# Kernel optimization log

Hardware: AMD Instinct MI355X
Metric: run time of the kernel (lower is better)

## Reference

```python
import jax, jax.numpy as jnp
import numpy as np

N_NODES = 10000
N_EDGES = 320000
D = 256
VOCAB = 28
NEG_SLOPE = 0.2


def _gat_conv(x, ei_src, ei_dst, W, a_src, a_dst, b):
    """PyG GATConv with heads=1, concat=True, self-loops already in ei."""
    h = x @ W                                  # [N, D]
    alpha_s = h @ a_src                        # [N]
    alpha_d = h @ a_dst                        # [N]
    logits = jax.nn.leaky_relu(alpha_s[ei_src] + alpha_d[ei_dst], NEG_SLOPE)  # [E]
    # numerically stable edge softmax per destination node
    m = jax.ops.segment_max(logits, ei_dst, num_segments=N_NODES)
    e = jnp.exp(logits - m[ei_dst])
    denom = jax.ops.segment_sum(e, ei_dst, num_segments=N_NODES)
    alpha = e / denom[ei_dst]                  # [E]
    msgs = alpha[:, None] * h[ei_src]          # [E, D]
    out = jax.ops.segment_sum(msgs, ei_dst, num_segments=N_NODES)
    return out + b


def setup_inputs() -> dict:
    key = jax.random.key(0)
    ks = jax.random.split(key, 16)
    x = jax.random.randint(ks[0], (N_NODES, 1), 0, VOCAB, dtype=jnp.int64)
    edge_index = jax.random.randint(ks[1], (2, N_EDGES), 0, N_NODES, dtype=jnp.int64)
    edge_attr = jax.random.uniform(ks[2], (N_EDGES,), dtype=jnp.float32)
    sc = 1.0 / np.sqrt(D)
    inp = {"x": x, "edge_index": edge_index, "edge_attr": edge_attr,
           "emb": jax.random.normal(ks[3], (VOCAB, D), jnp.float32)}
    for i, k0 in enumerate([4, 7, 10]):
        l = i + 1
        inp[f"W{l}"] = jax.random.normal(ks[k0], (D, D), jnp.float32) * sc
        inp[f"a_src{l}"] = jax.random.normal(ks[k0 + 1], (D,), jnp.float32) * sc
        inp[f"a_dst{l}"] = jax.random.normal(ks[k0 + 2], (D,), jnp.float32) * sc
        inp[f"b{l}"] = jnp.zeros((D,), jnp.float32)
    return inp


def reference(x, edge_index, edge_attr, emb,
              W1, a_src1, a_dst1, b1,
              W2, a_src2, a_dst2, b2,
              W3, a_src3, a_dst3, b3):
    # edge_attr is ignored by GATConv (edge_dim=None), matching PyG behavior.
    # add self loops (PyG default add_self_loops=True)
    loops = jnp.arange(N_NODES, dtype=edge_index.dtype)
    ei_src = jnp.concatenate([edge_index[0], loops])
    ei_dst = jnp.concatenate([edge_index[1], loops])

    h = emb[x.squeeze(-1)]                     # [N, D]
    h = jax.nn.relu(_gat_conv(h, ei_src, ei_dst, W1, a_src1, a_dst1, b1)) + h
    h = jax.nn.relu(_gat_conv(h, ei_src, ei_dst, W2, a_src2, a_dst2, b2)) + h
    out = jax.nn.relu(_gat_conv(h, ei_src, ei_dst, W3, a_src3, a_dst3, b3)) + h
    return out
```

## Files before the change

kernel.cpp:

```cpp
#include <hip/hip_runtime.h>
#include <hip/hip_bf16.h>

#define N_NODES 10000
#define N_EDGES 320000
#define E_TOT (N_EDGES + N_NODES)
#define D 256
#define VOCAB 28
#define NEG 0.2f
#define CAP 96

typedef __attribute__((ext_vector_type(8))) short bf16x8;
typedef __attribute__((ext_vector_type(4))) float f32x4;

__device__ inline float blo(unsigned u) { return __uint_as_float(u << 16); }
__device__ inline float bhi(unsigned u) { return __uint_as_float(u & 0xFFFF0000u); }
__device__ inline unsigned short f2bu(float x) {
  __hip_bfloat16 b = __float2bfloat16(x);
  return *reinterpret_cast<unsigned short*>(&b);
}

__global__ __launch_bounds__(256) void prep_kernel(const float* __restrict__ W0,
                                                   const float* __restrict__ W1,
                                                   const float* __restrict__ W2,
                                                   const float* __restrict__ emb,
                                                   const float* __restrict__ as1,
                                                   const float* __restrict__ ad1,
                                                   const float* __restrict__ as2,
                                                   const float* __restrict__ ad2,
                                                   const float* __restrict__ as3,
                                                   const float* __restrict__ ad3,
                                                   const int* __restrict__ x,
                                                   unsigned short* __restrict__ T0,
                                                   unsigned short* __restrict__ T1,
                                                   unsigned short* __restrict__ T2,
                                                   unsigned short* __restrict__ emb_b,
                                                   float4* __restrict__ zbase,
                                                   float* __restrict__ waS2,
                                                   float* __restrict__ waD2,
                                                   float* __restrict__ waS3,
                                                   float* __restrict__ waD3,
                                                   float* __restrict__ al1_s,
                                                   float* __restrict__ al1_d) {
  int tid = threadIdx.x;
  int bid = blockIdx.x;
  if (bid < 48) {
    __shared__ float t[64][65];
    int l = bid >> 4;
    const float* W = (l == 0) ? W0 : (l == 1) ? W1 : W2;
    unsigned short* Wt = (l == 0) ? T0 : (l == 1) ? T1 : T2;
    int sub = bid & 15;
    int bk = (sub & 3) * 64;
    int bn = (sub >> 2) * 64;
    int row = tid >> 2;
    int cq = (tid & 3) * 16;
#pragma unroll
    for (int i = 0; i < 4; ++i) {
      float4 v = *reinterpret_cast<const float4*>(W + (size_t)(bk + row) * D + bn + cq + i * 4);
      t[row][cq + i * 4 + 0] = v.x; t[row][cq + i * 4 + 1] = v.y;
      t[row][cq + i * 4 + 2] = v.z; t[row][cq + i * 4 + 3] = v.w;
    }
    __syncthreads();
#pragma unroll
    for (int i = 0; i < 16; ++i)
      Wt[(size_t)(bn + row) * D + bk + cq + i] = f2bu(t[cq + i][row]);
  } else if (bid == 48) {
    for (int i = tid; i < VOCAB * D; i += 256) emb_b[i] = f2bu(emb[i]);
  } else if (bid < 59) {
    zbase[(bid - 49) * 256 + tid] = float4{0.f, 0.f, 0.f, 0.f};
  } else if (bid == 59 || bid == 60) {
    const float* W = (bid == 59) ? W1 : W2;
    const float* as = (bid == 59) ? as2 : as3;
    const float* ad = (bid == 59) ? ad2 : ad3;
    float* oS = (bid == 59) ? waS2 : waS3;
    float* oD = (bid == 59) ? waD2 : waD3;
    float s = 0.f, d = 0.f;
    const float* row = W + (size_t)tid * D;
    for (int n = 0; n < D; ++n) {
      float w = row[n];
      s += w * as[n];
      d += w * ad[n];
    }
    oS[tid] = s; oD[tid] = d;
  } else {
    __shared__ float ws1[256], wd1[256], avs[VOCAB], avd[VOCAB];
    {
      float s = 0.f, d = 0.f;
      const float* row = W0 + (size_t)tid * D;
      for (int n = 0; n < D; ++n) {
        float w = row[n];
        s += w * as1[n];
        d += w * ad1[n];
      }
      ws1[tid] = s; wd1[tid] = d;
    }
    __syncthreads();
    int wid = tid >> 6, lane = tid & 63;
    for (int t = wid; t < VOCAB; t += 4) {
      float ps = 0.f, pd = 0.f;
      for (int k = lane; k < D; k += 64) {
        float e = emb[(size_t)t * D + k];
        ps += e * ws1[k];
        pd += e * wd1[k];
      }
#pragma unroll
      for (int off = 32; off; off >>= 1) {
        ps += __shfl_xor(ps, off);
        pd += __shfl_xor(pd, off);
      }
      if (lane == 0) { avs[t] = ps; avd[t] = pd; }
    }
    __syncthreads();
    for (int n = tid; n < N_NODES; n += 256) {
      int t = x[n];
      al1_s[n] = avs[t];
      al1_d[n] = avd[t];
    }
  }
}

__global__ __launch_bounds__(256) void scatter_kernel(const int* __restrict__ ei,
                                                      int* __restrict__ counts,
                                                      int* __restrict__ csr) {
  int e = blockIdx.x * 256 + threadIdx.x;
  if (e >= E_TOT) return;
  int src, dst;
  if (e < N_EDGES) { src = ei[e]; dst = ei[N_EDGES + e]; }
  else             { src = e - N_EDGES; dst = src; }
  int pos = atomicAdd(&counts[dst], 1);
  csr[dst * CAP + pos] = src;
}

__global__ __launch_bounds__(256) void gemm_kernel(const unsigned short* __restrict__ Asrc,
                                                   const int* __restrict__ xv,
                                                   const unsigned short* __restrict__ emb_b,
                                                   const unsigned short* __restrict__ Bt,
                                                   unsigned short* __restrict__ C) {
  __shared__ unsigned short As[64][72];
  __shared__ unsigned short Bs[64][72];
  __shared__ int xs[64];
  int t = threadIdx.x;
  int bm = blockIdx.x * 64;
  int bn = blockIdx.y * 64;
  int lane = t & 63, wid = t >> 6;
  int wr = (wid >> 1) * 32, wc = (wid & 1) * 32;
  int fr = lane & 15, fk = (lane >> 4) * 8;

  if (xv) {
    if (t < 64) {
      int gr = bm + t;
      xs[t] = (gr < N_NODES) ? xv[gr] : 0;
    }
    __syncthreads();
  }

  f32x4 acc[2][2] = {};
  for (int k0 = 0; k0 < D; k0 += 64) {
#pragma unroll
    for (int c = t; c < 512; c += 256) {
      int row = c >> 3, cc = (c & 7) * 8;
      int gr = bm + row;
      uint4 v = {0u, 0u, 0u, 0u};
      if (gr < N_NODES) {
        const unsigned short* src = xv ? (emb_b + (size_t)xs[row] * D)
                                       : (Asrc + (size_t)gr * D);
        v = *reinterpret_cast<const uint4*>(src + k0 + cc);
      }
      *reinterpret_cast<uint4*>(&As[row][cc]) = v;
      uint4 w = *reinterpret_cast<const uint4*>(Bt + (size_t)(bn + row) * D + k0 + cc);
      *reinterpret_cast<uint4*>(&Bs[row][cc]) = w;
    }
    __syncthreads();
#pragma unroll
    for (int ks = 0; ks < 2; ++ks) {
      bf16x8 a0 = *reinterpret_cast<const bf16x8*>(&As[wr + fr][ks * 32 + fk]);
      bf16x8 a1 = *reinterpret_cast<const bf16x8*>(&As[wr + 16 + fr][ks * 32 + fk]);
      bf16x8 b0 = *reinterpret_cast<const bf16x8*>(&Bs[wc + fr][ks * 32 + fk]);
      bf16x8 b1 = *reinterpret_cast<const bf16x8*>(&Bs[wc + 16 + fr][ks * 32 + fk]);
      acc[0][0] = __builtin_amdgcn_mfma_f32_16x16x32_bf16(a0, b0, acc[0][0], 0, 0, 0);
      acc[0][1] = __builtin_amdgcn_mfma_f32_16x16x32_bf16(a0, b1, acc[0][1], 0, 0, 0);
      acc[1][0] = __builtin_amdgcn_mfma_f32_16x16x32_bf16(a1, b0, acc[1][0], 0, 0, 0);
      acc[1][1] = __builtin_amdgcn_mfma_f32_16x16x32_bf16(a1, b1, acc[1][1], 0, 0, 0);
    }
    __syncthreads();
  }

  int orow = (lane >> 4) * 4;
#pragma unroll
  for (int m = 0; m < 2; ++m)
#pragma unroll
    for (int n = 0; n < 2; ++n)
#pragma unroll
      for (int r = 0; r < 4; ++r) {
        int gr = bm + wr + m * 16 + orow + r;
        if (gr < N_NODES)
          C[(size_t)gr * D + bn + wc + n * 16 + fr] = f2bu(acc[m][n][r]);
      }
}

__global__ __launch_bounds__(256) void agg_kernel(const int* __restrict__ csr,
                                                  const int* __restrict__ counts,
                                                  const float* __restrict__ al_s,
                                                  const float* __restrict__ al_d,
                                                  const unsigned short* __restrict__ hlin,
                                                  const float* __restrict__ bias,
                                                  const float* __restrict__ h_prev,
                                                  const int* __restrict__ xv,
                                                  const float* __restrict__ emb,
                                                  float* __restrict__ out_f,
                                                  unsigned short* __restrict__ out_b,
                                                  const float* __restrict__ waS_n,
                                                  const float* __restrict__ waD_n,
                                                  float* __restrict__ aln_s,
                                                  float* __restrict__ aln_d) {
  __shared__ int   ssh[4][CAP];
  __shared__ float wsh[4][CAP];
  int wid = threadIdx.x >> 6, lane = threadIdx.x & 63;
  int dst = blockIdx.x * 4 + wid;
  if (dst >= N_NODES) return;
  int cnt = counts[dst];
  const int* rowp = csr + (size_t)dst * CAP;
  float ad = al_d[dst];

  float m = -1e30f;
  for (int j = lane; j < cnt; j += 64) {
    int s = rowp[j];
    ssh[wid][j] = s;
    float v = al_s[s] + ad;
    v = (v >= 0.f) ? v : NEG * v;
    wsh[wid][j] = v;
    m = fmaxf(m, v);
  }
#pragma unroll
  for (int off = 32; off; off >>= 1) m = fmaxf(m, __shfl_xor(m, off));

  float denom = 0.f;
  for (int j = lane; j < cnt; j += 64) {
    float w = __expf(wsh[wid][j] - m);
    wsh[wid][j] = w;
    denom += w;
  }
#pragma unroll
  for (int off = 32; off; off >>= 1) denom += __shfl_xor(denom, off);
  float inv = 1.0f / denom;

  int half = lane >> 5, fl = lane & 31;
  const unsigned short* hb_base = hlin + fl * 8;
  float a0 = 0.f, a1 = 0.f, a2 = 0.f, a3 = 0.f;
  float a4 = 0.f, a5 = 0.f, a6 = 0.f, a7 = 0.f;
  int j = 0;
  for (; j + 8 <= cnt; j += 8) {
    int s0 = ssh[wid][j + 0 + half];
    int s1 = ssh[wid][j + 2 + half];
    int s2 = ssh[wid][j + 4 + half];
    int s3 = ssh[wid][j + 6 + half];
    float w0 = wsh[wid][j + 0 + half];
    float w1 = wsh[wid][j + 2 + half];
    float w2 = wsh[wid][j + 4 + half];
    float w3 = wsh[wid][j + 6 + half];
    uint4 q0 = *reinterpret_cast<const uint4*>(hb_base + (size_t)s0 * D);
    uint4 q1 = *reinterpret_cast<const uint4*>(hb_base + (size_t)s1 * D);
    uint4 q2 = *reinterpret_cast<const uint4*>(hb_base + (size_t)s2 * D);
    uint4 q3 = *reinterpret_cast<const uint4*>(hb_base + (size_t)s3 * D);
    a0 += w0 * blo(q0.x); a1 += w0 * bhi(q0.x); a2 += w0 * blo(q0.y); a3 += w0 * bhi(q0.y);
    a4 += w0 * blo(q0.z); a5 += w0 * bhi(q0.z); a6 += w0 * blo(q0.w); a7 += w0 * bhi(q0.w);
    a0 += w1 * blo(q1.x); a1 += w1 * bhi(q1.x); a2 += w1 * blo(q1.y); a3 += w1 * bhi(q1.y);
    a4 += w1 * blo(q1.z); a5 += w1 * bhi(q1.z); a6 += w1 * blo(q1.w); a7 += w1 * bhi(q1.w);
    a0 += w2 * blo(q2.x); a1 += w2 * bhi(q2.x); a2 += w2 * blo(q2.y); a3 += w2 * bhi(q2.y);
    a4 += w2 * blo(q2.z); a5 += w2 * bhi(q2.z); a6 += w2 * blo(q2.w); a7 += w2 * bhi(q2.w);
    a0 += w3 * blo(q3.x); a1 += w3 * bhi(q3.x); a2 += w3 * blo(q3.y); a3 += w3 * bhi(q3.y);
    a4 += w3 * blo(q3.z); a5 += w3 * bhi(q3.z); a6 += w3 * blo(q3.w); a7 += w3 * bhi(q3.w);
  }
  for (; j < cnt; j += 2) {
    int jj = j + half;
    bool valid = jj < cnt;
    int s0 = ssh[wid][valid ? jj : 0];
    float w0 = valid ? wsh[wid][jj] : 0.f;
    uint4 q0 = *reinterpret_cast<const uint4*>(hb_base + (size_t)s0 * D);
    a0 += w0 * blo(q0.x); a1 += w0 * bhi(q0.x); a2 += w0 * blo(q0.y); a3 += w0 * bhi(q0.y);
    a4 += w0 * blo(q0.z); a5 += w0 * bhi(q0.z); a6 += w0 * blo(q0.w); a7 += w0 * bhi(q0.w);
  }
  a0 += __shfl_xor(a0, 32); a1 += __shfl_xor(a1, 32);
  a2 += __shfl_xor(a2, 32); a3 += __shfl_xor(a3, 32);
  a4 += __shfl_xor(a4, 32); a5 += __shfl_xor(a5, 32);
  a6 += __shfl_xor(a6, 32); a7 += __shfl_xor(a7, 32);
  float b0 = half ? a4 : a0, b1 = half ? a5 : a1;
  float b2 = half ? a6 : a2, b3 = half ? a7 : a3;
  int fb = fl * 8 + half * 4;
  const float* hp_row = h_prev ? (h_prev + (size_t)dst * D)
                               : (emb + (size_t)xv[dst] * D);
  float4 bb = *reinterpret_cast<const float4*>(bias + fb);
  float4 hp = *reinterpret_cast<const float4*>(hp_row + fb);
  float o0 = fmaxf(b0 * inv + bb.x, 0.f) + hp.x;
  float o1 = fmaxf(b1 * inv + bb.y, 0.f) + hp.y;
  float o2 = fmaxf(b2 * inv + bb.z, 0.f) + hp.z;
  float o3 = fmaxf(b3 * inv + bb.w, 0.f) + hp.w;
  float4 o = {o0, o1, o2, o3};
  *reinterpret_cast<float4*>(out_f + (size_t)dst * D + fb) = o;
  if (out_b) {
    uint2 p;
    p.x = (unsigned)f2bu(o0) | ((unsigned)f2bu(o1) << 16);
    p.y = (unsigned)f2bu(o2) | ((unsigned)f2bu(o3) << 16);
    *reinterpret_cast<uint2*>(out_b + (size_t)dst * D + fb) = p;
  }
  if (waS_n) {
    float4 s4 = *reinterpret_cast<const float4*>(waS_n + fb);
    float4 d4 = *reinterpret_cast<const float4*>(waD_n + fb);
    float ps = o0 * s4.x + o1 * s4.y + o2 * s4.z + o3 * s4.w;
    float pd = o0 * d4.x + o1 * d4.y + o2 * d4.z + o3 * d4.w;
#pragma unroll
    for (int off = 32; off; off >>= 1) {
      ps += __shfl_xor(ps, off);
      pd += __shfl_xor(pd, off);
    }
    if (lane == 0) { aln_s[dst] = ps; aln_d[dst] = pd; }
  }
}

extern "C" void kernel_launch(void* const* d_in, const int* in_sizes, int n_in,
                              void* d_out, int out_size, void* d_ws, size_t ws_size,
                              hipStream_t stream) {
  const int*   x   = (const int*)d_in[0];
  const int*   ei  = (const int*)d_in[1];
  const float* emb = (const float*)d_in[3];
  const float* W[3]    = {(const float*)d_in[4],  (const float*)d_in[8],  (const float*)d_in[12]};
  const float* asrc[3] = {(const float*)d_in[5],  (const float*)d_in[9],  (const float*)d_in[13]};
  const float* adst[3] = {(const float*)d_in[6],  (const float*)d_in[10], (const float*)d_in[14]};
  const float* bias[3] = {(const float*)d_in[7],  (const float*)d_in[11], (const float*)d_in[15]};

  char* ws = (char*)d_ws;
  float*          h    = (float*)(ws);
  unsigned short* hb   = (unsigned short*)(ws + 10240000);
  unsigned short* hlin = (unsigned short*)(ws + 15360000);
  unsigned short* Wt[3] = {(unsigned short*)(ws + 20480000),
                           (unsigned short*)(ws + 20611072),
                           (unsigned short*)(ws + 20742144)};
  float* al_s[3] = {(float*)(ws + 20873216), (float*)(ws + 20914176), (float*)(ws + 20955136)};
  float* al_d[3] = {(float*)(ws + 20996096), (float*)(ws + 21037056), (float*)(ws + 21078016)};
  int* counts = (int*)(ws + 21118976);
  int* csr    = (int*)(ws + 21241856);
  unsigned short* emb_b = (unsigned short*)(ws + 25081856);
  float* waS2 = (float*)(ws + 25096192);
  float* waD2 = (float*)(ws + 25097216);
  float* waS3 = (float*)(ws + 25098240);
  float* waD3 = (float*)(ws + 25099264);

  prep_kernel<<<62, 256, 0, stream>>>(W[0], W[1], W[2], emb,
                                      asrc[0], adst[0], asrc[1], adst[1], asrc[2], adst[2],
                                      x, Wt[0], Wt[1], Wt[2], emb_b,
                                      (float4*)counts, waS2, waD2, waS3, waD3,
                                      al_s[0], al_d[0]);

  scatter_kernel<<<(E_TOT + 255) / 256, 256, 0, stream>>>(ei, counts, csr);

  dim3 gemm_grid(157, 4);
  for (int l = 0; l < 3; ++l) {
    const unsigned short* Ain = (l == 0) ? (const unsigned short*)nullptr : hb;
    const int* xg = (l == 0) ? x : (const int*)nullptr;
    gemm_kernel<<<gemm_grid, 256, 0, stream>>>(Ain, xg, emb_b, Wt[l], hlin);
    float* outp = (l == 2) ? (float*)d_out : h;
    unsigned short* outb = (l == 2) ? (unsigned short*)nullptr : hb;
    const float* hp = (l == 0) ? (const float*)nullptr : h;
    const float* wsn = (l == 0) ? waS2 : (l == 1) ? waS3 : (const float*)nullptr;
    const float* wdn = (l == 0) ? waD2 : (l == 1) ? waD3 : (const float*)nullptr;
    float* alns = (l < 2) ? al_s[l + 1] : (float*)nullptr;
    float* alnd = (l < 2) ? al_d[l + 1] : (float*)nullptr;
    agg_kernel<<<(N_NODES + 3) / 4, 256, 0, stream>>>(csr, counts, al_s[l], al_d[l],
                                                      hlin, bias[l], hp, x, emb,
                                                      outp, outb, wsn, wdn, alns, alnd);
  }
}
```

Baseline: 135.1 us.

## Aggregate before linear transform and fuse GEMM with residual and attention epilogue

Uses linearity of the attention-weighted sum to swap the order of work in each layer. Each layer now aggregates the bf16 input features first, and in layer one it gathers straight from the 28-row embedding table. A single full-width GEMM per 64-row tile then applies bias, ReLU and the residual, and computes the next layer's attention projections in its epilogue. The goals are cache-friendly gathers in the first layer and no round trip of the separate linear output through memory. In exchange the GEMM runs with only 157 blocks, uses large LDS tiles and writes scalar outputs, and the rounding order of the bf16 steps changes.

```diff
diff --git a/kernel.cpp b/kernel.cpp
--- a/kernel.cpp
+++ b/kernel.cpp
@@ -130,88 +130,13 @@
   csr[dst * CAP + pos] = src;
 }
 
-__global__ __launch_bounds__(256) void gemm_kernel(const unsigned short* __restrict__ Asrc,
+__global__ __launch_bounds__(256) void aggz_kernel(const int* __restrict__ csr,
+                                                   const int* __restrict__ counts,
+                                                   const float* __restrict__ al_s,
+                                                   const float* __restrict__ al_d,
+                                                   const unsigned short* __restrict__ table,
                                                    const int* __restrict__ xv,
-                                                   const unsigned short* __restrict__ emb_b,
-                                                   const unsigned short* __restrict__ Bt,
-                                                   unsigned short* __restrict__ C) {
-  __shared__ unsigned short As[64][72];
-  __shared__ unsigned short Bs[64][72];
-  __shared__ int xs[64];
-  int t = threadIdx.x;
-  int bm = blockIdx.x * 64;
-  int bn = blockIdx.y * 64;
-  int lane = t & 63, wid = t >> 6;
-  int wr = (wid >> 1) * 32, wc = (wid & 1) * 32;
-  int fr = lane & 15, fk = (lane >> 4) * 8;
-
-  if (xv) {
-    if (t < 64) {
-      int gr = bm + t;
-      xs[t] = (gr < N_NODES) ? xv[gr] : 0;
-    }
-    __syncthreads();
-  }
-
-  f32x4 acc[2][2] = {};
-  for (int k0 = 0; k0 < D; k0 += 64) {
-#pragma unroll
-    for (int c = t; c < 512; c += 256) {
-      int row = c >> 3, cc = (c & 7) * 8;
-      int gr = bm + row;
-      uint4 v = {0u, 0u, 0u, 0u};
-      if (gr < N_NODES) {
-        const unsigned short* src = xv ? (emb_b + (size_t)xs[row] * D)
-                                       : (Asrc + (size_t)gr * D);
-        v = *reinterpret_cast<const uint4*>(src + k0 + cc);
-      }
-      *reinterpret_cast<uint4*>(&As[row][cc]) = v;
-      uint4 w = *reinterpret_cast<const uint4*>(Bt + (size_t)(bn + row) * D + k0 + cc);
-      *reinterpret_cast<uint4*>(&Bs[row][cc]) = w;
-    }
-    __syncthreads();
-#pragma unroll
-    for (int ks = 0; ks < 2; ++ks) {
-      bf16x8 a0 = *reinterpret_cast<const bf16x8*>(&As[wr + fr][ks * 32 + fk]);
-      bf16x8 a1 = *reinterpret_cast<const bf16x8*>(&As[wr + 16 + fr][ks * 32 + fk]);
-      bf16x8 b0 = *reinterpret_cast<const bf16x8*>(&Bs[wc + fr][ks * 32 + fk]);
-      bf16x8 b1 = *reinterpret_cast<const bf16x8*>(&Bs[wc + 16 + fr][ks * 32 + fk]);
-      acc[0][0] = __builtin_amdgcn_mfma_f32_16x16x32_bf16(a0, b0, acc[0][0], 0, 0, 0);
-      acc[0][1] = __builtin_amdgcn_mfma_f32_16x16x32_bf16(a0, b1, acc[0][1], 0, 0, 0);
-      acc[1][0] = __builtin_amdgcn_mfma_f32_16x16x32_bf16(a1, b0, acc[1][0], 0, 0, 0);
-      acc[1][1] = __builtin_amdgcn_mfma_f32_16x16x32_bf16(a1, b1, acc[1][1], 0, 0, 0);
-    }
-    __syncthreads();
-  }
-
-  int orow = (lane >> 4) * 4;
-#pragma unroll
-  for (int m = 0; m < 2; ++m)
-#pragma unroll
-    for (int n = 0; n < 2; ++n)
-#pragma unroll
-      for (int r = 0; r < 4; ++r) {
-        int gr = bm + wr + m * 16 + orow + r;
-        if (gr < N_NODES)
-          C[(size_t)gr * D + bn + wc + n * 16 + fr] = f2bu(acc[m][n][r]);
-      }
-}
-
-__global__ __launch_bounds__(256) void agg_kernel(const int* __restrict__ csr,
-                                                  const int* __restrict__ counts,
-                                                  const float* __restrict__ al_s,
-                                                  const float* __restrict__ al_d,
-                                                  const unsigned short* __restrict__ hlin,
-                                                  const float* __restrict__ bias,
-                                                  const float* __restrict__ h_prev,
-                                                  const int* __restrict__ xv,
-                                                  const float* __restrict__ emb,
-                                                  float* __restrict__ out_f,
-                                                  unsigned short* __restrict__ out_b,
-                                                  const float* __restrict__ waS_n,
-                                                  const float* __restrict__ waD_n,
-                                                  float* __restrict__ aln_s,
-                                                  float* __restrict__ aln_d) {
+                                                   unsigned short* __restrict__ zb) {
   __shared__ int   ssh[4][CAP];
   __shared__ float wsh[4][CAP];
   int wid = threadIdx.x >> 6, lane = threadIdx.x & 63;
@@ -224,9 +149,9 @@
   float m = -1e30f;
   for (int j = lane; j < cnt; j += 64) {
     int s = rowp[j];
-    ssh[wid][j] = s;
     float v = al_s[s] + ad;
     v = (v >= 0.f) ? v : NEG * v;
+    ssh[wid][j] = xv ? xv[s] : s;
     wsh[wid][j] = v;
     m = fmaxf(m, v);
   }
@@ -244,7 +169,7 @@
   float inv = 1.0f / denom;
 
   int half = lane >> 5, fl = lane & 31;
-  const unsigned short* hb_base = hlin + fl * 8;
+  const unsigned short* hb_base = table + fl * 8;
   float a0 = 0.f, a1 = 0.f, a2 = 0.f, a3 = 0.f;
   float a4 = 0.f, a5 = 0.f, a6 = 0.f, a7 = 0.f;
   int j = 0;
@@ -286,33 +211,132 @@
   float b0 = half ? a4 : a0, b1 = half ? a5 : a1;
   float b2 = half ? a6 : a2, b3 = half ? a7 : a3;
   int fb = fl * 8 + half * 4;
-  const float* hp_row = h_prev ? (h_prev + (size_t)dst * D)
-                               : (emb + (size_t)xv[dst] * D);
-  float4 bb = *reinterpret_cast<const float4*>(bias + fb);
-  float4 hp = *reinterpret_cast<const float4*>(hp_row + fb);
-  float o0 = fmaxf(b0 * inv + bb.x, 0.f) + hp.x;
-  float o1 = fmaxf(b1 * inv + bb.y, 0.f) + hp.y;
-  float o2 = fmaxf(b2 * inv + bb.z, 0.f) + hp.z;
-  float o3 = fmaxf(b3 * inv + bb.w, 0.f) + hp.w;
-  float4 o = {o0, o1, o2, o3};
-  *reinterpret_cast<float4*>(out_f + (size_t)dst * D + fb) = o;
-  if (out_b) {
-    uint2 p;
-    p.x = (unsigned)f2bu(o0) | ((unsigned)f2bu(o1) << 16);
-    p.y = (unsigned)f2bu(o2) | ((unsigned)f2bu(o3) << 16);
-    *reinterpret_cast<uint2*>(out_b + (size_t)dst * D + fb) = p;
-  }
+  uint2 p;
+  p.x = (unsigned)f2bu(b0 * inv) | ((unsigned)f2bu(b1 * inv) << 16);
+  p.y = (unsigned)f2bu(b2 * inv) | ((unsigned)f2bu(b3 * inv) << 16);
+  *reinterpret_cast<uint2*>(zb + (size_t)dst * D + fb) = p;
+}
+
+__global__ __launch_bounds__(256) void gemmf_kernel(const unsigned short* __restrict__ Az,
+                                                    const unsigned short* __restrict__ Bt,
+                                                    const float* __restrict__ bias,
+                                                    const float* __restrict__ h_prev,
+                                                    const int* __restrict__ xv,
+                                                    const float* __restrict__ emb,
+                                                    float* __restrict__ h_out,
+                                                    unsigned short* __restrict__ hb_out,
+                                                    const float* __restrict__ waS_n,
+                                                    const float* __restrict__ waD_n,
+                                                    float* __restrict__ aln_s,
+                                                    float* __restrict__ aln_d) {
+  __shared__ unsigned short As[64][264];
+  __shared__ unsigned short Bs[64][264];
+  __shared__ float red_s[8][32];
+  __shared__ float red_d[8][32];
+  __shared__ int xs[64];
+  int t = threadIdx.x;
+  int bm = blockIdx.x * 64;
+  int lane = t & 63, wid = t >> 6;
+  int wrb = (wid >> 1) * 32, wcb = (wid & 1) * 32;
+  int fr = lane & 15, fk = (lane >> 4) * 8;
+  int orow = (lane >> 4) * 4;
+
+  if (xv) {
+    if (t < 64) {
+      int gr = bm + t;
+      xs[t] = (gr < N_NODES) ? xv[gr] : 0;
+    }
+    __syncthreads();
+  }
+
+#pragma unroll
+  for (int c = t; c < 2048; c += 256) {
+    int row = c >> 5, cc = (c & 31) * 8;
+    int gr = bm + row;
+    uint4 v = {0u, 0u, 0u, 0u};
+    if (gr < N_NODES)
+      v = *reinterpret_cast<const uint4*>(Az + (size_t)gr * D + cc);
+    *reinterpret_cast<uint4*>(&As[row][cc]) = v;
+  }
+
+  float aS[2][4] = {}, aD[2][4] = {};
+  for (int bn = 0; bn < 4; ++bn) {
+#pragma unroll
+    for (int c = t; c < 2048; c += 256) {
+      int row = c >> 5, cc = (c & 31) * 8;
+      uint4 w = *reinterpret_cast<const uint4*>(Bt + (size_t)(bn * 64 + row) * D + cc);
+      *reinterpret_cast<uint4*>(&Bs[row][cc]) = w;
+    }
+    __syncthreads();
+
+    f32x4 acc[2][2] = {};
+#pragma unroll
+    for (int ks = 0; ks < 8; ++ks) {
+      bf16x8 a0 = *reinterpret_cast<const bf16x8*>(&As[wrb + fr][ks * 32 + fk]);
+      bf16x8 a1 = *reinterpret_cast<const bf16x8*>(&As[wrb + 16 + fr][ks * 32 + fk]);
+      bf16x8 b0 = *reinterpret_cast<const bf16x8*>(&Bs[wcb + fr][ks * 32 + fk]);
+      bf16x8 b1 = *reinterpret_cast<const bf16x8*>(&Bs[wcb + 16 + fr][ks * 32 + fk]);
+      acc[0][0] = __builtin_amdgcn_mfma_f32_16x16x32_bf16(a0, b0, acc[0][0], 0, 0, 0);
+      acc[0][1] = __builtin_amdgcn_mfma_f32_16x16x32_bf16(a0, b1, acc[0][1], 0, 0, 0);
+      acc[1][0] = __builtin_amdgcn_mfma_f32_16x16x32_bf16(a1, b0, acc[1][0], 0, 0, 0);
+      acc[1][1] = __builtin_amdgcn_mfma_f32_16x16x32_bf16(a1, b1, acc[1][1], 0, 0, 0);
+    }
+
+    int c0 = bn * 64 + wcb + fr, c1 = c0 + 16;
+    float bb0 = bias[c0], bb1 = bias[c1];
+    float ws0 = 0.f, ws1 = 0.f, wd0 = 0.f, wd1 = 0.f;
+    if (waS_n) {
+      ws0 = waS_n[c0]; ws1 = waS_n[c1];
+      wd0 = waD_n[c0]; wd1 = waD_n[c1];
+    }
+#pragma unroll
+    for (int m = 0; m < 2; ++m)
+#pragma unroll
+      for (int r = 0; r < 4; ++r) {
+        int ri = wrb + m * 16 + orow + r;
+        int gr = bm + ri;
+        if (gr < N_NODES) {
+          const float* res = xv ? (emb + (size_t)xs[ri] * D) : (h_prev + (size_t)gr * D);
+          float v0 = fmaxf(acc[m][0][r] + bb0, 0.f) + res[c0];
+          float v1 = fmaxf(acc[m][1][r] + bb1, 0.f) + res[c1];
+          h_out[(size_t)gr * D + c0] = v0;
+          h_out[(size_t)gr * D + c1] = v1;
+          if (hb_out) {
+            hb_out[(size_t)gr * D + c0] = f2bu(v0);
+            hb_out[(size_t)gr * D + c1] = f2bu(v1);
+          }
+          aS[m][r] += v0 * ws0 + v1 * ws1;
+          aD[m][r] += v0 * wd0 + v1 * wd1;
+        }
+      }
+    __syncthreads();
+  }
+
   if (waS_n) {
-    float4 s4 = *reinterpret_cast<const float4*>(waS_n + fb);
-    float4 d4 = *reinterpret_cast<const float4*>(waD_n + fb);
-    float ps = o0 * s4.x + o1 * s4.y + o2 * s4.z + o3 * s4.w;
-    float pd = o0 * d4.x + o1 * d4.y + o2 * d4.z + o3 * d4.w;
-#pragma unroll
-    for (int off = 32; off; off >>= 1) {
-      ps += __shfl_xor(ps, off);
-      pd += __shfl_xor(pd, off);
-    }
-    if (lane == 0) { aln_s[dst] = ps; aln_d[dst] = pd; }
+#pragma unroll
+    for (int m = 0; m < 2; ++m)
+#pragma unroll
+      for (int r = 0; r < 4; ++r) {
+        float vs = aS[m][r], vd = aD[m][r];
+#pragma unroll
+        for (int off = 8; off; off >>= 1) {
+          vs += __shfl_xor(vs, off);
+          vd += __shfl_xor(vd, off);
+        }
+        if (fr == 0) {
+          red_s[wid][m * 16 + orow + r] = vs;
+          red_d[wid][m * 16 + orow + r] = vd;
+        }
+      }
+    __syncthreads();
+    if (t < 64) {
+      int gr = bm + t;
+      if (gr < N_NODES) {
+        int p = (t >> 5) * 2, lr = t & 31;
+        aln_s[gr] = red_s[p][lr] + red_s[p + 1][lr];
+        aln_d[gr] = red_d[p][lr] + red_d[p + 1][lr];
+      }
+    }
   }
 }
 
@@ -330,7 +354,7 @@
   char* ws = (char*)d_ws;
   float*          h    = (float*)(ws);
   unsigned short* hb   = (unsigned short*)(ws + 10240000);
-  unsigned short* hlin = (unsigned short*)(ws + 15360000);
+  unsigned short* zb   = (unsigned short*)(ws + 15360000);
   unsigned short* Wt[3] = {(unsigned short*)(ws + 20480000),
                            (unsigned short*)(ws + 20611072),
                            (unsigned short*)(ws + 20742144)};
@@ -352,20 +376,14 @@
 
   scatter_kernel<<<(E_TOT + 255) / 256, 256, 0, stream>>>(ei, counts, csr);
 
-  dim3 gemm_grid(157, 4);
-  for (int l = 0; l < 3; ++l) {
-    const unsigned short* Ain = (l == 0) ? (const unsigned short*)nullptr : hb;
-    const int* xg = (l == 0) ? x : (const int*)nullptr;
-    gemm_kernel<<<gemm_grid, 256, 0, stream>>>(Ain, xg, emb_b, Wt[l], hlin);
-    float* outp = (l == 2) ? (float*)d_out : h;
-    unsigned short* outb = (l == 2) ? (unsigned short*)nullptr : hb;
-    const float* hp = (l == 0) ? (const float*)nullptr : h;
-    const float* wsn = (l == 0) ? waS2 : (l == 1) ? waS3 : (const float*)nullptr;
-    const float* wdn = (l == 0) ? waD2 : (l == 1) ? waD3 : (const float*)nullptr;
-    float* alns = (l < 2) ? al_s[l + 1] : (float*)nullptr;
-    float* alnd = (l < 2) ? al_d[l + 1] : (float*)nullptr;
-    agg_kernel<<<(N_NODES + 3) / 4, 256, 0, stream>>>(csr, counts, al_s[l], al_d[l],
-                                                      hlin, bias[l], hp, x, emb,
-                                                      outp, outb, wsn, wdn, alns, alnd);
-  }
-}
+  aggz_kernel<<<2500, 256, 0, stream>>>(csr, counts, al_s[0], al_d[0], emb_b, x, zb);
+  gemmf_kernel<<<157, 256, 0, stream>>>(zb, Wt[0], bias[0], nullptr, x, emb,
+                                        h, hb, waS2, waD2, al_s[1], al_d[1]);
+  aggz_kernel<<<2500, 256, 0, stream>>>(csr, counts, al_s[1], al_d[1], hb, nullptr, zb);
+  gemmf_kernel<<<157, 256, 0, stream>>>(zb, Wt[1], bias[1], h, nullptr, nullptr,
+                                        h, hb, waS3, waD3, al_s[2], al_d[2]);
+  aggz_kernel<<<2500, 256, 0, stream>>>(csr, counts, al_s[2], al_d[2], hb, nullptr, zb);
+  gemmf_kernel<<<157, 256, 0, stream>>>(zb, Wt[2], bias[2], h, nullptr, nullptr,
+                                        (float*)d_out, nullptr, nullptr, nullptr,
+                                        nullptr, nullptr);
+}
```

After: 163.8 us. 21.3% more time.

## Precompute layer-1 linear transform per vocabulary token and gather in aggregation

Applied to the files above, without the earlier changes.

Layer 1's input rows are embedding lookups from a 28-token vocabulary, so x@W1 is computed once per token (28x256 table) in the prep kernel. The first GEMM launch is dropped, and the first aggregation gathers from the token table via an index indirection. This removes a 10000x256x256 GEMM and its launch, at the cost of an extra indexed load per edge in layer 1 and a naive per-token dot product in prep.

```diff
diff --git a/kernel.cpp b/kernel.cpp
--- a/kernel.cpp
+++ b/kernel.cpp
@@ -30,10 +30,9 @@
                                                    const float* __restrict__ as3,
                                                    const float* __restrict__ ad3,
                                                    const int* __restrict__ x,
-                                                   unsigned short* __restrict__ T0,
                                                    unsigned short* __restrict__ T1,
                                                    unsigned short* __restrict__ T2,
-                                                   unsigned short* __restrict__ emb_b,
+                                                   unsigned short* __restrict__ hv,
                                                    float4* __restrict__ zbase,
                                                    float* __restrict__ waS2,
                                                    float* __restrict__ waD2,
@@ -43,11 +42,11 @@
                                                    float* __restrict__ al1_d) {
   int tid = threadIdx.x;
   int bid = blockIdx.x;
-  if (bid < 48) {
+  if (bid < 32) {
     __shared__ float t[64][65];
     int l = bid >> 4;
-    const float* W = (l == 0) ? W0 : (l == 1) ? W1 : W2;
-    unsigned short* Wt = (l == 0) ? T0 : (l == 1) ? T1 : T2;
+    const float* W = (l == 0) ? W1 : W2;
+    unsigned short* Wt = (l == 0) ? T1 : T2;
     int sub = bid & 15;
     int bk = (sub & 3) * 64;
     int bn = (sub >> 2) * 64;
@@ -63,16 +62,14 @@
 #pragma unroll
     for (int i = 0; i < 16; ++i)
       Wt[(size_t)(bn + row) * D + bk + cq + i] = f2bu(t[cq + i][row]);
-  } else if (bid == 48) {
-    for (int i = tid; i < VOCAB * D; i += 256) emb_b[i] = f2bu(emb[i]);
-  } else if (bid < 59) {
-    zbase[(bid - 49) * 256 + tid] = float4{0.f, 0.f, 0.f, 0.f};
-  } else if (bid == 59 || bid == 60) {
-    const float* W = (bid == 59) ? W1 : W2;
-    const float* as = (bid == 59) ? as2 : as3;
-    const float* ad = (bid == 59) ? ad2 : ad3;
-    float* oS = (bid == 59) ? waS2 : waS3;
-    float* oD = (bid == 59) ? waD2 : waD3;
+  } else if (bid < 42) {
+    zbase[(bid - 32) * 256 + tid] = float4{0.f, 0.f, 0.f, 0.f};
+  } else if (bid == 42 || bid == 43) {
+    const float* W = (bid == 42) ? W1 : W2;
+    const float* as = (bid == 42) ? as2 : as3;
+    const float* ad = (bid == 42) ? ad2 : ad3;
+    float* oS = (bid == 42) ? waS2 : waS3;
+    float* oD = (bid == 42) ? waD2 : waD3;
     float s = 0.f, d = 0.f;
     const float* row = W + (size_t)tid * D;
     for (int n = 0; n < D; ++n) {
@@ -81,7 +78,7 @@
       d += w * ad[n];
     }
     oS[tid] = s; oD[tid] = d;
-  } else {
+  } else if (bid == 44) {
     __shared__ float ws1[256], wd1[256], avs[VOCAB], avd[VOCAB];
     {
       float s = 0.f, d = 0.f;
@@ -115,6 +112,12 @@
       al1_s[n] = avs[t];
       al1_d[n] = avd[t];
     }
+  } else {
+    int tok = bid - 45;
+    float s = 0.f;
+    for (int k = 0; k < D; ++k)
+      s += emb[(size_t)tok * D + k] * W0[(size_t)k * D + tid];
+    hv[(size_t)tok * D + tid] = f2bu(s);
   }
 }
 
@@ -131,13 +134,10 @@
 }
 
 __global__ __launch_bounds__(256) void gemm_kernel(const unsigned short* __restrict__ Asrc,
-                                                   const int* __restrict__ xv,
-                                                   const unsigned short* __restrict__ emb_b,
                                                    const unsigned short* __restrict__ Bt,
                                                    unsigned short* __restrict__ C) {
   __shared__ unsigned short As[64][72];
   __shared__ unsigned short Bs[64][72];
-  __shared__ int xs[64];
   int t = threadIdx.x;
   int bm = blockIdx.x * 64;
   int bn = blockIdx.y * 64;
@@ -145,14 +145,6 @@
   int wr = (wid >> 1) * 32, wc = (wid & 1) * 32;
   int fr = lane & 15, fk = (lane >> 4) * 8;
 
-  if (xv) {
-    if (t < 64) {
-      int gr = bm + t;
-      xs[t] = (gr < N_NODES) ? xv[gr] : 0;
-    }
-    __syncthreads();
-  }
-
   f32x4 acc[2][2] = {};
   for (int k0 = 0; k0 < D; k0 += 64) {
 #pragma unroll
@@ -160,11 +152,8 @@
       int row = c >> 3, cc = (c & 7) * 8;
       int gr = bm + row;
       uint4 v = {0u, 0u, 0u, 0u};
-      if (gr < N_NODES) {
-        const unsigned short* src = xv ? (emb_b + (size_t)xs[row] * D)
-                                       : (Asrc + (size_t)gr * D);
-        v = *reinterpret_cast<const uint4*>(src + k0 + cc);
-      }
+      if (gr < N_NODES)
+        v = *reinterpret_cast<const uint4*>(Asrc + (size_t)gr * D + k0 + cc);
       *reinterpret_cast<uint4*>(&As[row][cc]) = v;
       uint4 w = *reinterpret_cast<const uint4*>(Bt + (size_t)(bn + row) * D + k0 + cc);
       *reinterpret_cast<uint4*>(&Bs[row][cc]) = w;
@@ -211,7 +200,8 @@
                                                   const float* __restrict__ waS_n,
                                                   const float* __restrict__ waD_n,
                                                   float* __restrict__ aln_s,
-                                                  float* __restrict__ aln_d) {
+                                                  float* __restrict__ aln_d,
+                                                  const int* __restrict__ idx_tab) {
   __shared__ int   ssh[4][CAP];
   __shared__ float wsh[4][CAP];
   int wid = threadIdx.x >> 6, lane = threadIdx.x & 63;
@@ -224,7 +214,7 @@
   float m = -1e30f;
   for (int j = lane; j < cnt; j += 64) {
     int s = rowp[j];
-    ssh[wid][j] = s;
+    ssh[wid][j] = idx_tab ? idx_tab[s] : s;
     float v = al_s[s] + ad;
     v = (v >= 0.f) ? v : NEG * v;
     wsh[wid][j] = v;
@@ -331,41 +321,38 @@
   float*          h    = (float*)(ws);
   unsigned short* hb   = (unsigned short*)(ws + 10240000);
   unsigned short* hlin = (unsigned short*)(ws + 15360000);
-  unsigned short* Wt[3] = {(unsigned short*)(ws + 20480000),
-                           (unsigned short*)(ws + 20611072),
-                           (unsigned short*)(ws + 20742144)};
+  unsigned short* Wt1  = (unsigned short*)(ws + 20480000);
+  unsigned short* Wt2  = (unsigned short*)(ws + 20611072);
   float* al_s[3] = {(float*)(ws + 20873216), (float*)(ws + 20914176), (float*)(ws + 20955136)};
   float* al_d[3] = {(float*)(ws + 20996096), (float*)(ws + 21037056), (float*)(ws + 21078016)};
   int* counts = (int*)(ws + 21118976);
   int* csr    = (int*)(ws + 21241856);
-  unsigned short* emb_b = (unsigned short*)(ws + 25081856);
+  unsigned short* hv = (unsigned short*)(ws + 25081856);
   float* waS2 = (float*)(ws + 25096192);
   float* waD2 = (float*)(ws + 25097216);
   float* waS3 = (float*)(ws + 25098240);
   float* waD3 = (float*)(ws + 25099264);
 
-  prep_kernel<<<62, 256, 0, stream>>>(W[0], W[1], W[2], emb,
+  prep_kernel<<<73, 256, 0, stream>>>(W[0], W[1], W[2], emb,
                                       asrc[0], adst[0], asrc[1], adst[1], asrc[2], adst[2],
-                                      x, Wt[0], Wt[1], Wt[2], emb_b,
+                                      x, Wt1, Wt2, hv,
                                       (float4*)counts, waS2, waD2, waS3, waD3,
                                       al_s[0], al_d[0]);
 
   scatter_kernel<<<(E_TOT + 255) / 256, 256, 0, stream>>>(ei, counts, csr);
 
+  agg_kernel<<<2500, 256, 0, stream>>>(csr, counts, al_s[0], al_d[0],
+                                       hv, bias[0], nullptr, x, emb,
+                                       h, hb, waS2, waD2, al_s[1], al_d[1], x);
+
   dim3 gemm_grid(157, 4);
-  for (int l = 0; l < 3; ++l) {
-    const unsigned short* Ain = (l == 0) ? (const unsigned short*)nullptr : hb;
-    const int* xg = (l == 0) ? x : (const int*)nullptr;
-    gemm_kernel<<<gemm_grid, 256, 0, stream>>>(Ain, xg, emb_b, Wt[l], hlin);
-    float* outp = (l == 2) ? (float*)d_out : h;
-    unsigned short* outb = (l == 2) ? (unsigned short*)nullptr : hb;
-    const float* hp = (l == 0) ? (const float*)nullptr : h;
-    const float* wsn = (l == 0) ? waS2 : (l == 1) ? waS3 : (const float*)nullptr;
-    const float* wdn = (l == 0) ? waD2 : (l == 1) ? waD3 : (const float*)nullptr;
-    float* alns = (l < 2) ? al_s[l + 1] : (float*)nullptr;
-    float* alnd = (l < 2) ? al_d[l + 1] : (float*)nullptr;
-    agg_kernel<<<(N_NODES + 3) / 4, 256, 0, stream>>>(csr, counts, al_s[l], al_d[l],
-                                                      hlin, bias[l], hp, x, emb,
-                                                      outp, outb, wsn, wdn, alns, alnd);
-  }
-}
+  gemm_kernel<<<gemm_grid, 256, 0, stream>>>(hb, Wt1, hlin);
+  agg_kernel<<<2500, 256, 0, stream>>>(csr, counts, al_s[1], al_d[1],
+                                       hlin, bias[1], h, nullptr, nullptr,
+                                       h, hb, waS3, waD3, al_s[2], al_d[2], nullptr);
+  gemm_kernel<<<gemm_grid, 256, 0, stream>>>(hb, Wt2, hlin);
+  agg_kernel<<<2500, 256, 0, stream>>>(csr, counts, al_s[2], al_d[2],
+                                       hlin, bias[2], h, nullptr, nullptr,
+                                       (float*)d_out, nullptr, nullptr, nullptr,
+                                       nullptr, nullptr, nullptr);
+}
```

Result: faster. 118.6 us (median of 3 runs) (-12.2%).
